# Optimization experiments

Hardware: AMD Instinct MI355X
Metric: run time of the kernel (lower is better)

Reference implementation:

```python
import jax, jax.numpy as jnp
import numpy as np

B, T, C = 4, 1024, 768
NH, HS = 12, 64
V_SHIFT = 1
EXP_SCALE = 10.0
KB_UP = 5.0


def setup_inputs() -> dict:
    key = jax.random.key(0)
    ks = jax.random.split(key, 8)
    s = 1.0 / np.sqrt(C)
    x = jax.random.normal(ks[0], (B, T, C), dtype=jnp.float32)
    conv_w = jax.random.normal(ks[1], (C, C), dtype=jnp.float32) * s  # k featurizer 1x1 conv weight [out,in]
    lin_w = jax.random.normal(ks[2], (C, C), dtype=jnp.float32) * s   # v featurizer linear weight [out,in]
    coef = jax.random.uniform(ks[3], (NH,), dtype=jnp.float32)        # lowrlinearconv blend coef
    leaky_key_beta = (jnp.linspace(0.5, 5.0, NH) / EXP_SCALE).astype(jnp.float32)
    kernel_beta = (jnp.ones((NH,)) / EXP_SCALE).astype(jnp.float32)
    value_beta = (jnp.ones((NH,)) * (-0.5) / EXP_SCALE).astype(jnp.float32)
    proj_w = jax.random.normal(ks[4], (C, C), dtype=jnp.float32) * s  # c_proj weight [out,in]
    return {"x": x, "conv_w": conv_w, "lin_w": lin_w, "coef": coef,
            "leaky_key_beta": leaky_key_beta, "kernel_beta": kernel_beta,
            "value_beta": value_beta, "proj_w": proj_w}


def _split_heads(z):  # [B,T,C] -> [B,NH,T,HS]
    Bz, Tz, Cz = z.shape
    return z.reshape(Bz, Tz, NH, HS).transpose(0, 2, 1, 3)


def reference(x, conv_w, lin_w, coef, leaky_key_beta, kernel_beta, value_beta, proj_w):
    # --- k featurizer: 1x1 conv (pointwise linear), no norm ---
    k = _split_heads(jnp.einsum('btc,dc->btd', x, conv_w))  # [B,NH,T,HS]

    # --- v featurizer: linear, shift-left blend, per-head coef, L2 norm ---
    lin = jnp.einsum('btc,dc->btd', x, lin_w)               # [B,T,C]
    lin_s = jnp.concatenate([lin[:, 1:, :], jnp.zeros_like(lin[:, :1, :])], axis=1)
    vh, vs = _split_heads(lin), _split_heads(lin_s)
    c = coef[None, :, None, None]
    v = vs * (1.0 - c) + vh * c
    v = v / jnp.linalg.norm(v, axis=-1, keepdims=True)
    v = v * jnp.exp(value_beta * EXP_SCALE)[None, :, None, None]

    # --- leaky decay cumulative key averaging ---
    lkb = jnp.abs(leaky_key_beta) * EXP_SCALE                # [NH]
    d = jnp.arange(T)[:, None] - jnp.arange(T)[None, :]      # i - j
    lower = d >= 0
    decay = jnp.exp(-d[None].astype(jnp.float32) * lkb[:, None, None]) \
        * (1.0 - jnp.exp(-lkb))[:, None, None]               # [NH,T,T]
    decay = jnp.where(lower[None], decay, 0.0)
    k = jnp.einsum('hij,bhjd->bhid', decay, k)
    k = k / jnp.linalg.norm(k, axis=-1, keepdims=True)
    kb = jnp.exp(jnp.minimum(kernel_beta * EXP_SCALE, KB_UP))
    k = k * kb[None, :, None, None]

    # --- attention: k k^T with shifted causal mask, softmax ---
    att = jnp.einsum('bhid,bhjd->bhij', k, k)                # [B,NH,T,T]
    i_idx = jnp.arange(T)[:, None]
    j_idx = jnp.arange(T)[None, :]
    allowed = (j_idx <= i_idx - V_SHIFT)                     # [T,T]
    row_zero = (jnp.arange(T) < V_SHIFT)[:, None]            # rows set to 0
    scores = jnp.where(allowed | row_zero, jnp.where(allowed, att, 0.0), -jnp.inf)
    probs = jax.nn.softmax(scores, axis=-1)
    probs = jnp.where(row_zero[None, None], 0.0, probs)

    y = jnp.einsum('bhij,bhjd->bhid', probs, v)              # [B,NH,T,HS]
    y = y.transpose(0, 2, 1, 3).reshape(B, T, C)
    return jnp.einsum('btc,dc->btd', y, proj_w)
```

## Files before the change

kernel.cpp:

```cpp
#include <hip/hip_runtime.h>
#include <math.h>

#define B 4
#define T 1024
#define C 768
#define NH 12
#define HS 64
#define ESCALE 10.0f
#define KBUP 5.0f
#define ECH 64
#define NCH (T / ECH)

typedef short bf16x8 __attribute__((ext_vector_type(8)));
typedef short bf16x4v __attribute__((ext_vector_type(4)));
typedef float f32x4 __attribute__((ext_vector_type(4)));

__device__ inline unsigned short f2b(float f) {
  union { float f; unsigned int u; } x;
  x.f = f;
  unsigned int r = (x.u + 0x7FFF + ((x.u >> 16) & 1)) >> 16;
  return (unsigned short)r;
}
__device__ inline float b2f(unsigned short u) {
  union { float f; unsigned int i; } x;
  x.i = ((unsigned int)u) << 16;
  return x.f;
}

template <int MODE>
__global__ __launch_bounds__(256) void gemm_mfma(const void* __restrict__ Xp,
                                                 const float* __restrict__ W0,
                                                 const float* __restrict__ W1,
                                                 void* __restrict__ out0,
                                                 void* __restrict__ out1) {
  const int K = 768;
  __shared__ short sa_hi[128][40];
  __shared__ short sa_lo[(MODE == 0) ? 128 : 1][40];
  __shared__ short sb_hi[128][40];
  __shared__ short sb_lo[128][40];
  const int tid = threadIdx.x;
  const int m0 = blockIdx.x * 128;
  const int n0 = blockIdx.y * 128;
  const int w = tid >> 6, lane = tid & 63;
  const int wm = w >> 1, wn = w & 1;
  const int r16 = lane & 15, g = lane >> 4;
  const float* Wsel = (MODE == 0 && n0 >= 768) ? (W1 + (size_t)(n0 - 768) * K)
                                               : (W0 + (size_t)n0 * K);
  f32x4 acc[4][4];
#pragma unroll
  for (int mi = 0; mi < 4; ++mi)
#pragma unroll
    for (int ni = 0; ni < 4; ++ni) acc[mi][ni] = (f32x4){0.f, 0.f, 0.f, 0.f};

  for (int k0 = 0; k0 < K; k0 += 32) {
    __syncthreads();
#pragma unroll
    for (int i = 0; i < 4; ++i) {
      int row = (tid >> 3) + 32 * i;
      int c = tid & 7;
      float4 wv = *(const float4*)(Wsel + (size_t)row * K + k0 + c * 4);
      bf16x4v hi, lo;
      float vv[4] = {wv.x, wv.y, wv.z, wv.w};
#pragma unroll
      for (int e = 0; e < 4; ++e) {
        unsigned short h = f2b(vv[e]);
        hi[e] = (short)h;
        lo[e] = (short)f2b(vv[e] - b2f(h));
      }
      *(bf16x4v*)&sb_hi[row][c * 4] = hi;
      *(bf16x4v*)&sb_lo[row][c * 4] = lo;
    }
    if constexpr (MODE == 0) {
      const float* X = (const float*)Xp;
#pragma unroll
      for (int i = 0; i < 4; ++i) {
        int row = (tid >> 3) + 32 * i;
        int c = tid & 7;
        float4 xv = *(const float4*)(X + (size_t)(m0 + row) * K + k0 + c * 4);
        bf16x4v hi, lo;
        float vv[4] = {xv.x, xv.y, xv.z, xv.w};
#pragma unroll
        for (int e = 0; e < 4; ++e) {
          unsigned short h = f2b(vv[e]);
          hi[e] = (short)h;
          lo[e] = (short)f2b(vv[e] - b2f(h));
        }
        *(bf16x4v*)&sa_hi[row][c * 4] = hi;
        *(bf16x4v*)&sa_lo[row][c * 4] = lo;
      }
    } else {
      const unsigned short* X = (const unsigned short*)Xp;
#pragma unroll
      for (int i = 0; i < 2; ++i) {
        int row = (tid >> 2) + 64 * i;
        int c = tid & 3;
        *(bf16x8*)&sa_hi[row][c * 8] =
            *(const bf16x8*)(X + (size_t)(m0 + row) * K + k0 + c * 8);
      }
    }
    __syncthreads();
    bf16x8 ah[4], al[4], bh[4], bl[4];
#pragma unroll
    for (int mi = 0; mi < 4; ++mi) {
      ah[mi] = *(const bf16x8*)&sa_hi[wm * 64 + mi * 16 + r16][g * 8];
      if constexpr (MODE == 0)
        al[mi] = *(const bf16x8*)&sa_lo[wm * 64 + mi * 16 + r16][g * 8];
    }
#pragma unroll
    for (int ni = 0; ni < 4; ++ni) {
      bh[ni] = *(const bf16x8*)&sb_hi[wn * 64 + ni * 16 + r16][g * 8];
      bl[ni] = *(const bf16x8*)&sb_lo[wn * 64 + ni * 16 + r16][g * 8];
    }
#pragma unroll
    for (int mi = 0; mi < 4; ++mi)
#pragma unroll
      for (int ni = 0; ni < 4; ++ni) {
        acc[mi][ni] = __builtin_amdgcn_mfma_f32_16x16x32_bf16(ah[mi], bh[ni], acc[mi][ni], 0, 0, 0);
        acc[mi][ni] = __builtin_amdgcn_mfma_f32_16x16x32_bf16(ah[mi], bl[ni], acc[mi][ni], 0, 0, 0);
        if constexpr (MODE == 0)
          acc[mi][ni] = __builtin_amdgcn_mfma_f32_16x16x32_bf16(al[mi], bh[ni], acc[mi][ni], 0, 0, 0);
      }
  }
  if constexpr (MODE == 0) {
    if (n0 < 768) {
      unsigned short* ko = (unsigned short*)out0;
#pragma unroll
      for (int mi = 0; mi < 4; ++mi)
#pragma unroll
        for (int ni = 0; ni < 4; ++ni)
#pragma unroll
          for (int r = 0; r < 4; ++r) {
            int m = m0 + wm * 64 + mi * 16 + g * 4 + r;
            int n = n0 + wn * 64 + ni * 16 + r16;
            int bb = m >> 10, tt = m & 1023, h = n >> 6, d = n & 63;
            ko[(((size_t)(bb * NH + h)) * T + tt) * HS + d] = f2b(acc[mi][ni][r]);
          }
    } else {
      unsigned short* lo_ = (unsigned short*)out1;
#pragma unroll
      for (int mi = 0; mi < 4; ++mi)
#pragma unroll
        for (int ni = 0; ni < 4; ++ni)
#pragma unroll
          for (int r = 0; r < 4; ++r) {
            int m = m0 + wm * 64 + mi * 16 + g * 4 + r;
            int n = n0 + wn * 64 + ni * 16 + r16;
            lo_[(size_t)m * 768 + (n - 768)] = f2b(acc[mi][ni][r]);
          }
    }
  } else {
    float* oo = (float*)out0;
#pragma unroll
    for (int mi = 0; mi < 4; ++mi)
#pragma unroll
      for (int ni = 0; ni < 4; ++ni)
#pragma unroll
        for (int r = 0; r < 4; ++r) {
          int m = m0 + wm * 64 + mi * 16 + g * 4 + r;
          int n = n0 + wn * 64 + ni * 16 + r16;
          oo[(size_t)m * 768 + n] = acc[mi][ni][r];
        }
  }
}

__global__ __launch_bounds__(256) void vcompute(const unsigned short* __restrict__ lin,
                                                const float* __restrict__ coef,
                                                const float* __restrict__ vbeta,
                                                unsigned short* __restrict__ vout) {
  int w = (blockIdx.x * 256 + threadIdx.x) >> 6;
  int lane = threadIdx.x & 63;
  int t = w % T;
  int h = (w / T) % NH;
  int b = w / (T * NH);
  float c = coef[h];
  float vh = b2f(lin[((size_t)(b * T + t)) * C + h * HS + lane]);
  float vs = (t + 1 < T) ? b2f(lin[((size_t)(b * T + t + 1)) * C + h * HS + lane]) : 0.0f;
  float v = vs * (1.0f - c) + vh * c;
  float ss = v * v;
#pragma unroll
  for (int off = 1; off < 64; off <<= 1) ss += __shfl_xor(ss, off);
  float scale = rsqrtf(ss) * expf(vbeta[h] * ESCALE);
  vout[(((size_t)(b * NH + h) * T + t) * HS) + lane] = f2b(v * scale);
}

__global__ __launch_bounds__(64) void ema_scan(const unsigned short* __restrict__ kb,
                                               const float* __restrict__ lkb,
                                               float* __restrict__ ends) {
  const int bx = blockIdx.x;
  const int bh = bx >> 4, ch = bx & (NCH - 1);
  const int d = threadIdx.x;
  const int h = bh % NH;
  const float lam = fabsf(lkb[h]) * ESCALE;
  const float a = expf(-lam), wf = 1.0f - a;
  const unsigned short* p = kb + (size_t)bh * T * HS + d;
  const int t0 = ch * ECH;
  float s = 0.0f;
#pragma unroll 8
  for (int t = t0; t < t0 + ECH; ++t) s = a * s + wf * b2f(p[(size_t)t * HS]);
  ends[((size_t)bh * NCH + ch) * HS + d] = s;
}

__global__ __launch_bounds__(64) void ema_apply(unsigned short* __restrict__ kb,
                                                const float* __restrict__ lkb,
                                                const float* __restrict__ kbeta,
                                                const float* __restrict__ ends) {
  const int bx = blockIdx.x;
  const int bh = bx >> 4, ch = bx & (NCH - 1);
  const int d = threadIdx.x;
  const int h = bh % NH;
  const float lam = fabsf(lkb[h]) * ESCALE;
  const float a = expf(-lam), wf = 1.0f - a;
  const float a64 = expf(-lam * (float)ECH);
  const float kbs = expf(fminf(kbeta[h] * ESCALE, KBUP));
  unsigned short* p = kb + (size_t)bh * T * HS + d;
  float carry = 0.0f;
  for (int c = 0; c < ch; ++c)
    carry = a64 * carry + ends[((size_t)bh * NCH + c) * HS + d];
  float s = carry;
  const int t0 = ch * ECH;
  for (int tb = 0; tb < ECH; tb += 8) {
    float sr[8], q[8];
#pragma unroll
    for (int u = 0; u < 8; ++u) {
      s = a * s + wf * b2f(p[(size_t)(t0 + tb + u) * HS]);
      sr[u] = s;
    }
#pragma unroll
    for (int u = 0; u < 8; ++u) q[u] = sr[u] * sr[u];
#pragma unroll
    for (int off = 1; off < 64; off <<= 1)
#pragma unroll
      for (int u = 0; u < 8; ++u) q[u] += __shfl_xor(q[u], off);
#pragma unroll
    for (int u = 0; u < 8; ++u)
      p[(size_t)(t0 + tb + u) * HS] = f2b(sr[u] * rsqrtf(q[u]) * kbs);
  }
}

__global__ __launch_bounds__(256) void attn_mfma(const unsigned short* __restrict__ Km,
                                                 const unsigned short* __restrict__ Vm,
                                                 unsigned short* __restrict__ Y) {
  const int bid = blockIdx.x;
  const int qt = 15 - (bid / (B * NH));
  const int bh = bid % (B * NH);
  const int b = bh / NH, h = bh % NH;
  const int qi0 = qt * 64;
  const short* Kb = (const short*)(Km + (size_t)bh * T * HS);
  const short* Vb = (const short*)(Vm + (size_t)bh * T * HS);
  __shared__ short kt[64 * 72];
  __shared__ short vt[64 * 72];
  __shared__ short pl[4 * 16 * 72];
  const int tid = threadIdx.x;
  const int w = tid >> 6, lane = tid & 63;
  const int qr = lane & 15, qg = lane >> 4;

  bf16x8 qf0 = *(const bf16x8*)(Kb + (size_t)(qi0 + w * 16 + qr) * HS + qg * 8);
  bf16x8 qf1 = *(const bf16x8*)(Kb + (size_t)(qi0 + w * 16 + qr) * HS + qg * 8 + 32);

  f32x4 o[4];
#pragma unroll
  for (int db = 0; db < 4; ++db) o[db] = (f32x4){0.f, 0.f, 0.f, 0.f};
  float m_st = -INFINITY, l_st = 0.0f;

  const int njt = qt + 1;
  for (int jt = 0; jt < njt; ++jt) {
    const int j0 = jt * 64;
    __syncthreads();
#pragma unroll
    for (int it = 0; it < 2; ++it) {
      int idx = tid + it * 256;
      int row = idx >> 3, ch = idx & 7;
      *(bf16x8*)&kt[row * 72 + ch * 8] =
          *(const bf16x8*)(Kb + (size_t)(j0 + row) * HS + ch * 8);
      int vj = idx & 63, vd0 = (idx >> 6) * 8;
      bf16x8 vv = *(const bf16x8*)(Vb + (size_t)(j0 + vj) * HS + vd0);
#pragma unroll
      for (int e = 0; e < 8; ++e) vt[(vd0 + e) * 72 + vj] = vv[e];
    }
    __syncthreads();
    f32x4 st[4];
#pragma unroll
    for (int jb = 0; jb < 4; ++jb) st[jb] = (f32x4){0.f, 0.f, 0.f, 0.f};
#pragma unroll
    for (int jb = 0; jb < 4; ++jb) {
      bf16x8 kf0 = *(const bf16x8*)&kt[(qr + 16 * jb) * 72 + qg * 8];
      bf16x8 kf1 = *(const bf16x8*)&kt[(qr + 16 * jb) * 72 + qg * 8 + 32];
      st[jb] = __builtin_amdgcn_mfma_f32_16x16x32_bf16(kf0, qf0, st[jb], 0, 0, 0);
      st[jb] = __builtin_amdgcn_mfma_f32_16x16x32_bf16(kf1, qf1, st[jb], 0, 0, 0);
    }
    if (jt == njt - 1) {
      const int ii = qi0 + w * 16 + qr;
#pragma unroll
      for (int jb = 0; jb < 4; ++jb)
#pragma unroll
        for (int r = 0; r < 4; ++r) {
          int jj = j0 + 16 * jb + qg * 4 + r;
          if (jj >= ii) st[jb][r] = -INFINITY;
        }
    }
    float rm = -INFINITY;
#pragma unroll
    for (int jb = 0; jb < 4; ++jb)
#pragma unroll
      for (int r = 0; r < 4; ++r) rm = fmaxf(rm, st[jb][r]);
    rm = fmaxf(rm, __shfl_xor(rm, 16));
    rm = fmaxf(rm, __shfl_xor(rm, 32));
    float mnew = fmaxf(m_st, rm);
    float scale = (mnew == -INFINITY) ? 1.0f : __expf(m_st - mnew);
    float p[4][4];
    float rs = 0.0f;
#pragma unroll
    for (int jb = 0; jb < 4; ++jb)
#pragma unroll
      for (int r = 0; r < 4; ++r) {
        float pv = (st[jb][r] == -INFINITY) ? 0.0f : __expf(st[jb][r] - mnew);
        p[jb][r] = pv;
        rs += pv;
      }
    rs += __shfl_xor(rs, 16);
    rs += __shfl_xor(rs, 32);
    l_st = l_st * scale + rs;
    m_st = mnew;
#pragma unroll
    for (int db = 0; db < 4; ++db) o[db] *= scale;
#pragma unroll
    for (int jb = 0; jb < 4; ++jb) {
      bf16x4v pw;
#pragma unroll
      for (int r = 0; r < 4; ++r) pw[r] = (short)f2b(p[jb][r]);
      *(bf16x4v*)&pl[w * 1152 + qr * 72 + jb * 16 + qg * 4] = pw;
    }
#pragma unroll
    for (int ks = 0; ks < 2; ++ks) {
      bf16x8 pf = *(const bf16x8*)&pl[w * 1152 + qr * 72 + ks * 32 + qg * 8];
#pragma unroll
      for (int db = 0; db < 4; ++db) {
        bf16x8 vf = *(const bf16x8*)&vt[(qr + 16 * db) * 72 + qg * 8 + ks * 32];
        o[db] = __builtin_amdgcn_mfma_f32_16x16x32_bf16(vf, pf, o[db], 0, 0, 0);
      }
    }
  }
  float inv = (l_st > 0.0f) ? 1.0f / l_st : 0.0f;
#pragma unroll
  for (int db = 0; db < 4; ++db) {
    bf16x4v yv;
#pragma unroll
    for (int r = 0; r < 4; ++r) yv[r] = (short)f2b(o[db][r] * inv);
    *(bf16x4v*)(Y + (size_t)(b * T + qi0 + w * 16 + qr) * C + h * HS + db * 16 + qg * 4) = yv;
  }
}

extern "C" void kernel_launch(void* const* d_in, const int* in_sizes, int n_in,
                              void* d_out, int out_size, void* d_ws, size_t ws_size,
                              hipStream_t stream) {
  const float* x = (const float*)d_in[0];
  const float* conv_w = (const float*)d_in[1];
  const float* lin_w = (const float*)d_in[2];
  const float* coef = (const float*)d_in[3];
  const float* lkb = (const float*)d_in[4];
  const float* kbeta = (const float*)d_in[5];
  const float* vbeta = (const float*)d_in[6];
  const float* proj_w = (const float*)d_in[7];

  const size_t NE = (size_t)B * T * C;
  unsigned short* abuf = (unsigned short*)d_ws;
  unsigned short* kbuf = abuf + NE;
  unsigned short* vbuf = (unsigned short*)d_out;
  float* ends = (float*)(vbuf + NE);

  gemm_mfma<0><<<dim3(32, 12), 256, 0, stream>>>(x, conv_w, lin_w, kbuf, abuf);
  vcompute<<<(B * NH * T) / 4, 256, 0, stream>>>(abuf, coef, vbeta, vbuf);
  ema_scan<<<B * NH * NCH, 64, 0, stream>>>(kbuf, lkb, ends);
  ema_apply<<<B * NH * NCH, 64, 0, stream>>>(kbuf, lkb, kbeta, ends);
  attn_mfma<<<T / 64 * B * NH, 256, 0, stream>>>(kbuf, vbuf, abuf);
  gemm_mfma<1><<<dim3(32, 6), 256, 0, stream>>>(abuf, proj_w, nullptr, d_out, nullptr);
}
```

Baseline: 214.0 us.

## Pre-split x into bf16 hi/lo and halve GEMM M-tile to 64

```diff
diff --git a/kernel.cpp b/kernel.cpp
--- a/kernel.cpp
+++ b/kernel.cpp
@@ -27,38 +27,62 @@
   return x.f;
 }
 
+__global__ __launch_bounds__(256) void split_x(const float* __restrict__ x,
+                                               unsigned short* __restrict__ xhi,
+                                               unsigned short* __restrict__ xlo) {
+  const size_t NEl = (size_t)B * T * C;
+  size_t i = ((size_t)blockIdx.x * 256 + threadIdx.x) * 4;
+  const size_t stride = (size_t)gridDim.x * 256 * 4;
+  for (; i < NEl; i += stride) {
+    float4 v = *(const float4*)(x + i);
+    float vv[4] = {v.x, v.y, v.z, v.w};
+    ushort4 hi, lo;
+    unsigned short* hp = (unsigned short*)&hi;
+    unsigned short* lp = (unsigned short*)&lo;
+#pragma unroll
+    for (int e = 0; e < 4; ++e) {
+      unsigned short h = f2b(vv[e]);
+      hp[e] = h;
+      lp[e] = f2b(vv[e] - b2f(h));
+    }
+    *(ushort4*)(xhi + i) = hi;
+    *(ushort4*)(xlo + i) = lo;
+  }
+}
+
 template <int MODE>
-__global__ __launch_bounds__(256) void gemm_mfma(const void* __restrict__ Xp,
+__global__ __launch_bounds__(256) void gemm_mfma(const unsigned short* __restrict__ Xhi,
+                                                 const unsigned short* __restrict__ Xlo,
                                                  const float* __restrict__ W0,
                                                  const float* __restrict__ W1,
                                                  void* __restrict__ out0,
                                                  void* __restrict__ out1) {
   const int K = 768;
-  __shared__ short sa_hi[128][40];
-  __shared__ short sa_lo[(MODE == 0) ? 128 : 1][40];
+  __shared__ short sa_hi[64][40];
+  __shared__ short sa_lo[(MODE == 0) ? 64 : 1][40];
   __shared__ short sb_hi[128][40];
   __shared__ short sb_lo[128][40];
   const int tid = threadIdx.x;
-  const int m0 = blockIdx.x * 128;
+  const int m0 = blockIdx.x * 64;
   const int n0 = blockIdx.y * 128;
   const int w = tid >> 6, lane = tid & 63;
-  const int wm = w >> 1, wn = w & 1;
   const int r16 = lane & 15, g = lane >> 4;
+  const int arow = tid >> 2, ac = (tid & 3) * 8;
+  const int wrow = tid >> 3, wc = (tid & 7) * 4;
   const float* Wsel = (MODE == 0 && n0 >= 768) ? (W1 + (size_t)(n0 - 768) * K)
                                                : (W0 + (size_t)n0 * K);
-  f32x4 acc[4][4];
+  f32x4 acc[4][2];
 #pragma unroll
   for (int mi = 0; mi < 4; ++mi)
 #pragma unroll
-    for (int ni = 0; ni < 4; ++ni) acc[mi][ni] = (f32x4){0.f, 0.f, 0.f, 0.f};
+    for (int ni = 0; ni < 2; ++ni) acc[mi][ni] = (f32x4){0.f, 0.f, 0.f, 0.f};
 
   for (int k0 = 0; k0 < K; k0 += 32) {
     __syncthreads();
 #pragma unroll
     for (int i = 0; i < 4; ++i) {
-      int row = (tid >> 3) + 32 * i;
-      int c = tid & 7;
-      float4 wv = *(const float4*)(Wsel + (size_t)row * K + k0 + c * 4);
+      int row = wrow + 32 * i;
+      float4 wv = *(const float4*)(Wsel + (size_t)row * K + k0 + wc);
       bf16x4v hi, lo;
       float vv[4] = {wv.x, wv.y, wv.z, wv.w};
 #pragma unroll
@@ -67,54 +91,32 @@
         hi[e] = (short)h;
         lo[e] = (short)f2b(vv[e] - b2f(h));
       }
-      *(bf16x4v*)&sb_hi[row][c * 4] = hi;
-      *(bf16x4v*)&sb_lo[row][c * 4] = lo;
-    }
+      *(bf16x4v*)&sb_hi[row][wc] = hi;
+      *(bf16x4v*)&sb_lo[row][wc] = lo;
+    }
+    *(bf16x8*)&sa_hi[arow][ac] =
+        *(const bf16x8*)(Xhi + (size_t)(m0 + arow) * K + k0 + ac);
     if constexpr (MODE == 0) {
-      const float* X = (const float*)Xp;
-#pragma unroll
-      for (int i = 0; i < 4; ++i) {
-        int row = (tid >> 3) + 32 * i;
-        int c = tid & 7;
-        float4 xv = *(const float4*)(X + (size_t)(m0 + row) * K + k0 + c * 4);
-        bf16x4v hi, lo;
-        float vv[4] = {xv.x, xv.y, xv.z, xv.w};
-#pragma unroll
-        for (int e = 0; e < 4; ++e) {
-          unsigned short h = f2b(vv[e]);
-          hi[e] = (short)h;
-          lo[e] = (short)f2b(vv[e] - b2f(h));
-        }
-        *(bf16x4v*)&sa_hi[row][c * 4] = hi;
-        *(bf16x4v*)&sa_lo[row][c * 4] = lo;
-      }
-    } else {
-      const unsigned short* X = (const unsigned short*)Xp;
-#pragma unroll
-      for (int i = 0; i < 2; ++i) {
-        int row = (tid >> 2) + 64 * i;
-        int c = tid & 3;
-        *(bf16x8*)&sa_hi[row][c * 8] =
-            *(const bf16x8*)(X + (size_t)(m0 + row) * K + k0 + c * 8);
-      }
+      *(bf16x8*)&sa_lo[arow][ac] =
+          *(const bf16x8*)(Xlo + (size_t)(m0 + arow) * K + k0 + ac);
     }
     __syncthreads();
-    bf16x8 ah[4], al[4], bh[4], bl[4];
+    bf16x8 ah[4], al[4], bh[2], bl[2];
 #pragma unroll
     for (int mi = 0; mi < 4; ++mi) {
-      ah[mi] = *(const bf16x8*)&sa_hi[wm * 64 + mi * 16 + r16][g * 8];
+      ah[mi] = *(const bf16x8*)&sa_hi[mi * 16 + r16][g * 8];
       if constexpr (MODE == 0)
-        al[mi] = *(const bf16x8*)&sa_lo[wm * 64 + mi * 16 + r16][g * 8];
-    }
-#pragma unroll
-    for (int ni = 0; ni < 4; ++ni) {
-      bh[ni] = *(const bf16x8*)&sb_hi[wn * 64 + ni * 16 + r16][g * 8];
-      bl[ni] = *(const bf16x8*)&sb_lo[wn * 64 + ni * 16 + r16][g * 8];
+        al[mi] = *(const bf16x8*)&sa_lo[mi * 16 + r16][g * 8];
+    }
+#pragma unroll
+    for (int ni = 0; ni < 2; ++ni) {
+      bh[ni] = *(const bf16x8*)&sb_hi[w * 32 + ni * 16 + r16][g * 8];
+      bl[ni] = *(const bf16x8*)&sb_lo[w * 32 + ni * 16 + r16][g * 8];
     }
 #pragma unroll
     for (int mi = 0; mi < 4; ++mi)
 #pragma unroll
-      for (int ni = 0; ni < 4; ++ni) {
+      for (int ni = 0; ni < 2; ++ni) {
         acc[mi][ni] = __builtin_amdgcn_mfma_f32_16x16x32_bf16(ah[mi], bh[ni], acc[mi][ni], 0, 0, 0);
         acc[mi][ni] = __builtin_amdgcn_mfma_f32_16x16x32_bf16(ah[mi], bl[ni], acc[mi][ni], 0, 0, 0);
         if constexpr (MODE == 0)
@@ -127,11 +129,11 @@
 #pragma unroll
       for (int mi = 0; mi < 4; ++mi)
 #pragma unroll
-        for (int ni = 0; ni < 4; ++ni)
+        for (int ni = 0; ni < 2; ++ni)
 #pragma unroll
           for (int r = 0; r < 4; ++r) {
-            int m = m0 + wm * 64 + mi * 16 + g * 4 + r;
-            int n = n0 + wn * 64 + ni * 16 + r16;
+            int m = m0 + mi * 16 + g * 4 + r;
+            int n = n0 + w * 32 + ni * 16 + r16;
             int bb = m >> 10, tt = m & 1023, h = n >> 6, d = n & 63;
             ko[(((size_t)(bb * NH + h)) * T + tt) * HS + d] = f2b(acc[mi][ni][r]);
           }
@@ -140,11 +142,11 @@
 #pragma unroll
       for (int mi = 0; mi < 4; ++mi)
 #pragma unroll
-        for (int ni = 0; ni < 4; ++ni)
+        for (int ni = 0; ni < 2; ++ni)
 #pragma unroll
           for (int r = 0; r < 4; ++r) {
-            int m = m0 + wm * 64 + mi * 16 + g * 4 + r;
-            int n = n0 + wn * 64 + ni * 16 + r16;
+            int m = m0 + mi * 16 + g * 4 + r;
+            int n = n0 + w * 32 + ni * 16 + r16;
             lo_[(size_t)m * 768 + (n - 768)] = f2b(acc[mi][ni][r]);
           }
     }
@@ -153,11 +155,11 @@
 #pragma unroll
     for (int mi = 0; mi < 4; ++mi)
 #pragma unroll
-      for (int ni = 0; ni < 4; ++ni)
+      for (int ni = 0; ni < 2; ++ni)
 #pragma unroll
         for (int r = 0; r < 4; ++r) {
-          int m = m0 + wm * 64 + mi * 16 + g * 4 + r;
-          int n = n0 + wn * 64 + ni * 16 + r16;
+          int m = m0 + mi * 16 + g * 4 + r;
+          int n = n0 + w * 32 + ni * 16 + r16;
           oo[(size_t)m * 768 + n] = acc[mi][ni][r];
         }
   }
@@ -365,13 +367,16 @@
   const size_t NE = (size_t)B * T * C;
   unsigned short* abuf = (unsigned short*)d_ws;
   unsigned short* kbuf = abuf + NE;
+  unsigned short* xhi = (unsigned short*)d_out;
+  unsigned short* xlo = xhi + NE;
   unsigned short* vbuf = (unsigned short*)d_out;
   float* ends = (float*)(vbuf + NE);
 
-  gemm_mfma<0><<<dim3(32, 12), 256, 0, stream>>>(x, conv_w, lin_w, kbuf, abuf);
+  split_x<<<2048, 256, 0, stream>>>(x, xhi, xlo);
+  gemm_mfma<0><<<dim3(64, 12), 256, 0, stream>>>(xhi, xlo, conv_w, lin_w, kbuf, abuf);
   vcompute<<<(B * NH * T) / 4, 256, 0, stream>>>(abuf, coef, vbeta, vbuf);
   ema_scan<<<B * NH * NCH, 64, 0, stream>>>(kbuf, lkb, ends);
   ema_apply<<<B * NH * NCH, 64, 0, stream>>>(kbuf, lkb, kbeta, ends);
   attn_mfma<<<T / 64 * B * NH, 256, 0, stream>>>(kbuf, vbuf, abuf);
-  gemm_mfma<1><<<dim3(32, 6), 256, 0, stream>>>(abuf, proj_w, nullptr, d_out, nullptr);
-}
+  gemm_mfma<1><<<dim3(64, 6), 256, 0, stream>>>(abuf, abuf, proj_w, nullptr, d_out, nullptr);
+}
```

After: 205.2 us. 4.1% less time.
